# Optimization experiments

Hardware: AMD Instinct MI355X
Metric: run time of the kernel (lower is better)

Reference implementation:

```python
import jax, jax.numpy as jnp
import numpy as np

N_DEG = 5
RANK = 4
SCALE = 4
IMW = IMH = 512
S = IMW * IMH
BATCH = 64
C_CH = 1


def setup_inputs() -> dict:
    key = jax.random.key(0)
    k1, k2, k3, k4 = jax.random.split(key, 4)
    x = jax.random.normal(k1, (BATCH, C_CH, IMW // SCALE, IMH // SCALE), dtype=jnp.float32)
    # CP-decomposed polynomial (CCP) factors; small init keeps degree-5 products stable
    A = jax.random.normal(k2, (N_DEG, RANK, S), dtype=jnp.float32) * 0.01
    C = jax.random.normal(k3, (S, RANK), dtype=jnp.float32) * 0.01
    b = jax.random.normal(k4, (S,), dtype=jnp.float32) * 0.01
    return {"x": x, "A": A, "C": C, "b": b}


def reference(x, A, C, b):
    bsize, c, w, h = x.shape
    # bilinear upsample, align_corners=False (half-pixel, matches torch default)
    up = jax.image.resize(x, (bsize, c, w * SCALE, h * SCALE), method="bilinear")
    flat = up.reshape(bsize, c, S)
    v = flat[:, c - 1, :]  # [B, S] -- original applies PolyLayer only to channel c-1
    # CCP polynomial network: z1 = A1 v; z_n = (A_n v) * z_{n-1} + z_{n-1}
    za = jnp.einsum("nrs,bs->bnr", A, v)  # [B, N, rank]
    z = za[:, 0]
    for n in range(1, N_DEG):
        z = za[:, n] * z + z
    out_v = jnp.einsum("br,sr->bs", z, C) + b  # [B, S]
    flat = flat.at[:, c - 1, :].set(out_v)
    return flat.reshape(bsize, c, w * SCALE, h * SCALE)
```

## Files before the change

### kernel.cpp

```cpp
#include <hip/hip_runtime.h>

#define S_TOTAL (512 * 512)
#define BATCH 64
#define KTOT 65536
#define KTOT2 16384

typedef float vfloat4 __attribute__((ext_vector_type(4)));

__device__ __forceinline__ float swz_x1(float v) {
    return __int_as_float(__builtin_amdgcn_ds_swizzle(__float_as_int(v), 0x041F));
}
__device__ __forceinline__ float swz_x2(float v) {
    return __int_as_float(__builtin_amdgcn_ds_swizzle(__float_as_int(v), 0x081F));
}
__device__ __forceinline__ float swz_x4(float v) {
    return __int_as_float(__builtin_amdgcn_ds_swizzle(__float_as_int(v), 0x101F));
}
__device__ __forceinline__ float swz_x8(float v) {
    return __int_as_float(__builtin_amdgcn_ds_swizzle(__float_as_int(v), 0x201F));
}

__global__ __launch_bounds__(256) void adjx_kernel(
    const float* __restrict__ A,
    float* __restrict__ B1)
{
    __shared__ float rows[1024];
    const int t = threadIdx.x;
    const size_t base = (size_t)blockIdx.x * 1024;
#pragma unroll
    for (int e = 0; e < 4; ++e) rows[t + 256 * e] = A[base + t + 256 * e];
    __syncthreads();

    const int r = t >> 7;
    const int j = t & 127;
    const float* Lr = &rows[r * 512];
    const int bidx = 4 * j - 2;
    const float w[8] = {0.125f, 0.375f, 0.625f, 0.875f,
                        0.875f, 0.625f, 0.375f, 0.125f};
    float s = 0.0f;
#pragma unroll
    for (int p = 0; p < 8; ++p) {
        const int ix = bidx + p;
        if (ix >= 0 && ix < 512) s = fmaf(w[p], Lr[ix], s);
    }
    if (j == 0)   s += 0.375f * Lr[0]   + 0.125f * Lr[1];
    if (j == 127) s += 0.125f * Lr[510] + 0.375f * Lr[511];

    B1[(size_t)blockIdx.x * 256 + t] = s;
}

__global__ __launch_bounds__(128) void adjy_kernel(
    const float* __restrict__ B1,
    float* __restrict__ B2)
{
    const int j  = threadIdx.x;
    const int ty = blockIdx.x & 127;
    const int nr = blockIdx.x >> 7;
    const float* Bn = B1 + (size_t)nr * KTOT;
    const int biy = 4 * ty - 2;
    const float w[8] = {0.125f, 0.375f, 0.625f, 0.875f,
                        0.875f, 0.625f, 0.375f, 0.125f};
    float s = 0.0f;
#pragma unroll
    for (int p = 0; p < 8; ++p) {
        const int iy = biy + p;
        if (iy >= 0 && iy < 512) s = fmaf(w[p], Bn[iy * 128 + j], s);
    }
    if (ty == 0)   s += 0.375f * Bn[j]             + 0.125f * Bn[128 + j];
    if (ty == 127) s += 0.125f * Bn[510 * 128 + j] + 0.375f * Bn[511 * 128 + j];

    B2[(size_t)nr * KTOT2 + ty * 128 + j] = s;
}

__global__ __launch_bounds__(512) void za_partial_kernel(
    const float* __restrict__ x,
    const float* __restrict__ B2,
    float* __restrict__ partial)
{
    const int t    = threadIdx.x;
    const int blk  = blockIdx.x;
    const int w    = t >> 6;
    const int lane = t & 63;
    const int b0   = w * 8;
    const size_t kbase = (size_t)blk * 256 + 4 * lane;

    vfloat4 xv[8];
#pragma unroll
    for (int bi = 0; bi < 8; ++bi)
        xv[bi] = *(const vfloat4*)(x + (size_t)(b0 + bi) * KTOT2 + kbase);

    float* pb = partial + (size_t)blk * 1280;
    const int lane1 = lane & 1, lane2 = lane & 2, lane4 = lane & 4, lane8 = lane & 8;

#pragma unroll
    for (int ch = 0; ch < 2; ++ch) {
        float acc[16][5];
#pragma unroll
        for (int v = 0; v < 16; ++v)
#pragma unroll
            for (int tt = 0; tt < 5; ++tt) acc[v][tt] = 0.0f;

#pragma unroll
        for (int tt = 0; tt < 5; ++tt)
#pragma unroll
            for (int par = 0; par < 2; ++par) {
                const int nr = ch * 10 + 2 * tt + par;
                const vfloat4 bq = *(const vfloat4*)(B2 + (size_t)nr * KTOT2 + kbase);
#pragma unroll
                for (int bi = 0; bi < 8; ++bi) {
                    acc[bi * 2 + par][tt] =
                        fmaf(bq.x, xv[bi].x, fmaf(bq.y, xv[bi].y,
                        fmaf(bq.z, xv[bi].z, fmaf(bq.w, xv[bi].w,
                             acc[bi * 2 + par][tt]))));
                }
            }

        float s1[8][5];
#pragma unroll
        for (int v = 0; v < 8; ++v)
#pragma unroll
            for (int tt = 0; tt < 5; ++tt) {
                const float u = acc[v][tt], h = acc[v + 8][tt];
                s1[v][tt] = (lane1 ? h : u) + swz_x1(lane1 ? u : h);
            }
        float s2[4][5];
#pragma unroll
        for (int v = 0; v < 4; ++v)
#pragma unroll
            for (int tt = 0; tt < 5; ++tt) {
                const float u = s1[v][tt], h = s1[v + 4][tt];
                s2[v][tt] = (lane2 ? h : u) + swz_x2(lane2 ? u : h);
            }
        float s3[2][5];
#pragma unroll
        for (int v = 0; v < 2; ++v)
#pragma unroll
            for (int tt = 0; tt < 5; ++tt) {
                const float u = s2[v][tt], h = s2[v + 2][tt];
                s3[v][tt] = (lane4 ? h : u) + swz_x4(lane4 ? u : h);
            }
        float s4[5];
#pragma unroll
        for (int tt = 0; tt < 5; ++tt) {
            const float u = s3[0][tt], h = s3[1][tt];
            s4[tt] = (lane8 ? h : u) + swz_x8(lane8 ? u : h);
        }
#pragma unroll
        for (int tt = 0; tt < 5; ++tt) {
            s4[tt] += __shfl_xor(s4[tt], 16, 64);
            s4[tt] += __shfl_xor(s4[tt], 32, 64);
        }

        if (lane < 16) {
            const int m = ((lane & 1) << 3) | ((lane & 2) << 1) |
                          ((lane & 4) >> 1) | ((lane & 8) >> 3);
            float* dst = pb + (b0 + (m >> 1)) * 20 + ch * 10 + (m & 1);
#pragma unroll
            for (int tt = 0; tt < 5; ++tt) dst[2 * tt] = s4[tt];
        }
    }
}

__global__ __launch_bounds__(256) void za_reduce_kernel(
    const float* __restrict__ partial, float* __restrict__ za)
{
    const int c = blockIdx.x * 256 + threadIdx.x;
    float a0 = 0, a1 = 0, a2 = 0, a3 = 0;
    for (int r = 0; r < 64; r += 4) {
        a0 += partial[(size_t)(r + 0) * 1280 + c];
        a1 += partial[(size_t)(r + 1) * 1280 + c];
        a2 += partial[(size_t)(r + 2) * 1280 + c];
        a3 += partial[(size_t)(r + 3) * 1280 + c];
    }
    za[c] = (a0 + a1) + (a2 + a3);
}

__global__ __launch_bounds__(256) void out_kernel(
    const float* __restrict__ C,
    const float* __restrict__ bias,
    const float* __restrict__ za,
    float* __restrict__ out)
{
    __shared__ float zs[BATCH][4];
    const int t = threadIdx.x;
    if (t < 64) {
#pragma unroll
        for (int r = 0; r < 4; ++r) {
            float zv = za[t * 20 + r];
#pragma unroll
            for (int n = 1; n < 5; ++n)
                zv *= (1.0f + za[t * 20 + n * 4 + r]);
            zs[t][r] = zv;
        }
    }
    __syncthreads();

    const int s0 = (blockIdx.x * 256 + t) * 4;
    const vfloat4 c0 = *(const vfloat4*)(C + (size_t)s0 * 4);
    const vfloat4 c1 = *(const vfloat4*)(C + (size_t)s0 * 4 + 4);
    const vfloat4 c2 = *(const vfloat4*)(C + (size_t)s0 * 4 + 8);
    const vfloat4 c3 = *(const vfloat4*)(C + (size_t)s0 * 4 + 12);
    const vfloat4 bv = *(const vfloat4*)(bias + s0);

#pragma unroll 8
    for (int bb = 0; bb < BATCH; ++bb) {
        const float z0 = zs[bb][0], z1 = zs[bb][1];
        const float z2 = zs[bb][2], z3 = zs[bb][3];
        vfloat4 o;
        o.x = fmaf(z0, c0.x, fmaf(z1, c0.y, fmaf(z2, c0.z, fmaf(z3, c0.w, bv.x))));
        o.y = fmaf(z0, c1.x, fmaf(z1, c1.y, fmaf(z2, c1.z, fmaf(z3, c1.w, bv.y))));
        o.z = fmaf(z0, c2.x, fmaf(z1, c2.y, fmaf(z2, c2.z, fmaf(z3, c2.w, bv.z))));
        o.w = fmaf(z0, c3.x, fmaf(z1, c3.y, fmaf(z2, c3.z, fmaf(z3, c3.w, bv.w))));
        __builtin_nontemporal_store(o, (vfloat4*)(out + (size_t)bb * S_TOTAL + s0));
    }
}

extern "C" void kernel_launch(void* const* d_in, const int* in_sizes, int n_in,
                              void* d_out, int out_size, void* d_ws, size_t ws_size,
                              hipStream_t stream)
{
    const float* x    = (const float*)d_in[0];
    const float* A    = (const float*)d_in[1];
    const float* C    = (const float*)d_in[2];
    const float* bias = (const float*)d_in[3];
    float* out = (float*)d_out;

    float* B1      = (float*)d_ws;
    float* B2      = B1 + (size_t)20 * KTOT;
    float* partial = B2 + (size_t)20 * KTOT2;
    float* za      = partial + (size_t)64 * 1280;

    adjx_kernel<<<5120, 256, 0, stream>>>(A, B1);
    adjy_kernel<<<2560, 128, 0, stream>>>(B1, B2);
    za_partial_kernel<<<64, 512, 0, stream>>>(x, B2, partial);
    za_reduce_kernel<<<5, 256, 0, stream>>>(partial, za);
    out_kernel<<<256, 256, 0, stream>>>(C, bias, za, out);
}
```

Measured before the change: 37.26 us.

## Fuse separable adjoint-resize passes into one tiled kernel; halve out_kernel work per thread

The x- and y-direction adjoint bilinear passes over A are merged into one kernel. Each block loads a 20-row halo strip of A into shared memory, does the horizontal reduction into a local buffer, then the vertical reduction, and writes B2 directly. This removes the B1 round trip through global memory and one launch, at the cost of re-reading four halo rows per 16-row tile. Separately, out_kernel now computes two outputs per thread over twice as many blocks, giving more parallelism and fewer registers per thread.

```diff
diff --git a/kernel.cpp b/kernel.cpp
--- a/kernel.cpp
+++ b/kernel.cpp
@@ -2,10 +2,10 @@
 
 #define S_TOTAL (512 * 512)
 #define BATCH 64
-#define KTOT 65536
 #define KTOT2 16384
 
 typedef float vfloat4 __attribute__((ext_vector_type(4)));
+typedef float vfloat2 __attribute__((ext_vector_type(2)));
 
 __device__ __forceinline__ float swz_x1(float v) {
     return __int_as_float(__builtin_amdgcn_ds_swizzle(__float_as_int(v), 0x041F));
@@ -20,56 +20,67 @@
     return __int_as_float(__builtin_amdgcn_ds_swizzle(__float_as_int(v), 0x201F));
 }
 
-__global__ __launch_bounds__(256) void adjx_kernel(
+__global__ __launch_bounds__(256) void adjxy_kernel(
     const float* __restrict__ A,
-    float* __restrict__ B1)
-{
-    __shared__ float rows[1024];
-    const int t = threadIdx.x;
-    const size_t base = (size_t)blockIdx.x * 1024;
-#pragma unroll
-    for (int e = 0; e < 4; ++e) rows[t + 256 * e] = A[base + t + 256 * e];
+    float* __restrict__ B2)
+{
+    __shared__ float arows[20][512];
+    __shared__ float b1loc[20][128];
+
+    const int t  = threadIdx.x;
+    const int nr = blockIdx.x >> 5;
+    const int tc = blockIdx.x & 31;
+    const int y0 = 16 * tc - 2;
+
+    const float* An = A + (size_t)nr * S_TOTAL;
+#pragma unroll
+    for (int i = t; i < 20 * 128; i += 256) {
+        const int rl = i >> 7;
+        const int q  = i & 127;
+        const int y  = y0 + rl;
+        vfloat4 v = {0.0f, 0.0f, 0.0f, 0.0f};
+        if (y >= 0 && y < 512)
+            v = *(const vfloat4*)(An + (size_t)y * 512 + q * 4);
+        *(vfloat4*)&arows[rl][q * 4] = v;
+    }
     __syncthreads();
 
-    const int r = t >> 7;
-    const int j = t & 127;
-    const float* Lr = &rows[r * 512];
-    const int bidx = 4 * j - 2;
+#pragma unroll
+    for (int i = t; i < 20 * 128; i += 256) {
+        const int rl = i >> 7;
+        const int j  = i & 127;
+        const int base = 4 * j;
+        const vfloat4 m0 = *(const vfloat4*)&arows[rl][max(base - 4, 0)];
+        const vfloat4 m1 = *(const vfloat4*)&arows[rl][base];
+        const vfloat4 m2 = *(const vfloat4*)&arows[rl][min(base + 4, 508)];
+        float e0 = m0.z, e1 = m0.w, e6 = m2.x, e7 = m2.y;
+        if (j == 0)   { e0 = 0.0f; e1 = 0.0f; }
+        if (j == 127) { e6 = 0.0f; e7 = 0.0f; }
+        float s = 0.125f * e0 + 0.375f * e1
+                + 0.625f * m1.x + 0.875f * m1.y
+                + 0.875f * m1.z + 0.625f * m1.w
+                + 0.375f * e6 + 0.125f * e7;
+        if (j == 0)   s += 0.375f * arows[rl][0]   + 0.125f * arows[rl][1];
+        if (j == 127) s += 0.125f * arows[rl][510] + 0.375f * arows[rl][511];
+        b1loc[rl][j] = s;
+    }
+    __syncthreads();
+
     const float w[8] = {0.125f, 0.375f, 0.625f, 0.875f,
                         0.875f, 0.625f, 0.375f, 0.125f};
-    float s = 0.0f;
-#pragma unroll
-    for (int p = 0; p < 8; ++p) {
-        const int ix = bidx + p;
-        if (ix >= 0 && ix < 512) s = fmaf(w[p], Lr[ix], s);
-    }
-    if (j == 0)   s += 0.375f * Lr[0]   + 0.125f * Lr[1];
-    if (j == 127) s += 0.125f * Lr[510] + 0.375f * Lr[511];
-
-    B1[(size_t)blockIdx.x * 256 + t] = s;
-}
-
-__global__ __launch_bounds__(128) void adjy_kernel(
-    const float* __restrict__ B1,
-    float* __restrict__ B2)
-{
-    const int j  = threadIdx.x;
-    const int ty = blockIdx.x & 127;
-    const int nr = blockIdx.x >> 7;
-    const float* Bn = B1 + (size_t)nr * KTOT;
-    const int biy = 4 * ty - 2;
-    const float w[8] = {0.125f, 0.375f, 0.625f, 0.875f,
-                        0.875f, 0.625f, 0.375f, 0.125f};
-    float s = 0.0f;
-#pragma unroll
-    for (int p = 0; p < 8; ++p) {
-        const int iy = biy + p;
-        if (iy >= 0 && iy < 512) s = fmaf(w[p], Bn[iy * 128 + j], s);
-    }
-    if (ty == 0)   s += 0.375f * Bn[j]             + 0.125f * Bn[128 + j];
-    if (ty == 127) s += 0.125f * Bn[510 * 128 + j] + 0.375f * Bn[511 * 128 + j];
-
-    B2[(size_t)nr * KTOT2 + ty * 128 + j] = s;
+#pragma unroll
+    for (int i = t; i < 512; i += 256) {
+        const int tyl = i >> 7;
+        const int j   = i & 127;
+        const int ty  = tc * 4 + tyl;
+        float s = 0.0f;
+#pragma unroll
+        for (int p = 0; p < 8; ++p)
+            s = fmaf(w[p], b1loc[4 * tyl + p][j], s);
+        if (ty == 0)   s += 0.375f * b1loc[2][j]  + 0.125f * b1loc[3][j];
+        if (ty == 127) s += 0.125f * b1loc[16][j] + 0.375f * b1loc[17][j];
+        B2[(size_t)nr * KTOT2 + ty * 128 + j] = s;
+    }
 }
 
 __global__ __launch_bounds__(512) void za_partial_kernel(
@@ -195,23 +206,19 @@
     }
     __syncthreads();
 
-    const int s0 = (blockIdx.x * 256 + t) * 4;
+    const int s0 = (blockIdx.x * 256 + t) * 2;
     const vfloat4 c0 = *(const vfloat4*)(C + (size_t)s0 * 4);
     const vfloat4 c1 = *(const vfloat4*)(C + (size_t)s0 * 4 + 4);
-    const vfloat4 c2 = *(const vfloat4*)(C + (size_t)s0 * 4 + 8);
-    const vfloat4 c3 = *(const vfloat4*)(C + (size_t)s0 * 4 + 12);
-    const vfloat4 bv = *(const vfloat4*)(bias + s0);
+    const vfloat2 bv = *(const vfloat2*)(bias + s0);
 
 #pragma unroll 8
     for (int bb = 0; bb < BATCH; ++bb) {
         const float z0 = zs[bb][0], z1 = zs[bb][1];
         const float z2 = zs[bb][2], z3 = zs[bb][3];
-        vfloat4 o;
+        vfloat2 o;
         o.x = fmaf(z0, c0.x, fmaf(z1, c0.y, fmaf(z2, c0.z, fmaf(z3, c0.w, bv.x))));
         o.y = fmaf(z0, c1.x, fmaf(z1, c1.y, fmaf(z2, c1.z, fmaf(z3, c1.w, bv.y))));
-        o.z = fmaf(z0, c2.x, fmaf(z1, c2.y, fmaf(z2, c2.z, fmaf(z3, c2.w, bv.z))));
-        o.w = fmaf(z0, c3.x, fmaf(z1, c3.y, fmaf(z2, c3.z, fmaf(z3, c3.w, bv.w))));
-        __builtin_nontemporal_store(o, (vfloat4*)(out + (size_t)bb * S_TOTAL + s0));
+        __builtin_nontemporal_store(o, (vfloat2*)(out + (size_t)bb * S_TOTAL + s0));
     }
 }
 
@@ -225,14 +232,12 @@
     const float* bias = (const float*)d_in[3];
     float* out = (float*)d_out;
 
-    float* B1      = (float*)d_ws;
-    float* B2      = B1 + (size_t)20 * KTOT;
+    float* B2      = (float*)d_ws;
     float* partial = B2 + (size_t)20 * KTOT2;
     float* za      = partial + (size_t)64 * 1280;
 
-    adjx_kernel<<<5120, 256, 0, stream>>>(A, B1);
-    adjy_kernel<<<2560, 128, 0, stream>>>(B1, B2);
+    adjxy_kernel<<<640, 256, 0, stream>>>(A, B2);
     za_partial_kernel<<<64, 512, 0, stream>>>(x, B2, partial);
     za_reduce_kernel<<<5, 256, 0, stream>>>(partial, za);
-    out_kernel<<<256, 256, 0, stream>>>(C, bias, za, out);
-}
+    out_kernel<<<512, 256, 0, stream>>>(C, bias, za, out);
+}
```

Result: faster. 35.87 us (-3.7%).
